# Kernel optimization log

Hardware: AMD Instinct MI355X
Metric: run time of the kernel (lower is better)

The kernel has to match this reference:

```python
import jax, jax.numpy as jnp
import numpy as np

N_NODES = 50000
N_EDGES = 1600000
BN_EPS = 1e-5


def gcn_conv(x, W, b, src, dst, n):
    # PyG GCNConv: h = x @ W; add self-loops; sym-normalized scatter-add; + bias
    h = x @ W                                   # [n, out]
    deg = jnp.zeros((n,), h.dtype).at[dst].add(1.0) + 1.0  # in-degree incl. self-loop
    dinv = jax.lax.rsqrt(deg)                   # deg^{-1/2}
    norm = dinv[src] * dinv[dst]                # per-edge norm
    msg = h[src] * norm[:, None]                # [E, out] gather + scale
    agg = jax.ops.segment_sum(msg, dst, num_segments=n)
    agg = agg + h * (dinv * dinv)[:, None]      # self-loop term: dinv[i]^2 * h[i]
    return agg + b


def bn_eval(x, gamma, beta, mean, var):
    return (x - mean) * jax.lax.rsqrt(var + BN_EPS) * gamma + beta


def setup_inputs() -> dict:
    key = jax.random.key(0)
    ks = jax.random.split(key, 10)
    in_f, c1, c2, out_f = 256, 128, 64, 2
    x = jax.random.normal(ks[0], (N_NODES, in_f), jnp.float32)
    edge_index = jax.random.randint(ks[1], (2, N_EDGES), 0, N_NODES, jnp.int64)
    return {
        "x": x,
        "edge_index": edge_index,
        "W1": jax.random.normal(ks[2], (in_f, c1), jnp.float32) * (1.0 / np.sqrt(in_f)),
        "b1": jnp.zeros((c1,), jnp.float32),
        "W2": jax.random.normal(ks[3], (c1, c2), jnp.float32) * (1.0 / np.sqrt(c1)),
        "b2": jnp.zeros((c2,), jnp.float32),
        "bn1_gamma": jnp.ones((c1,), jnp.float32),
        "bn1_beta": jnp.zeros((c1,), jnp.float32),
        "bn1_mean": jax.random.normal(ks[4], (c1,), jnp.float32) * 0.1,
        "bn1_var": jax.random.uniform(ks[5], (c1,), jnp.float32) + 0.5,
        "bn2_gamma": jnp.ones((c2,), jnp.float32),
        "bn2_beta": jnp.zeros((c2,), jnp.float32),
        "bn2_mean": jax.random.normal(ks[6], (c2,), jnp.float32) * 0.1,
        "bn2_var": jax.random.uniform(ks[7], (c2,), jnp.float32) + 0.5,
        "Wl": jax.random.normal(ks[8], (c2, out_f), jnp.float32) * (1.0 / np.sqrt(c2)),
        "bl": jnp.zeros((out_f,), jnp.float32),
    }


def reference(x, edge_index, W1, b1, W2, b2, bn1_gamma, bn1_beta, bn1_mean, bn1_var,
              bn2_gamma, bn2_beta, bn2_mean, bn2_var, Wl, bl):
    src, dst = edge_index[0], edge_index[1]
    n = x.shape[0]
    h = jax.nn.relu(gcn_conv(x, W1, b1, src, dst, n))
    h = bn_eval(h, bn1_gamma, bn1_beta, bn1_mean, bn1_var)
    # dropout: eval mode -> identity
    h = jax.nn.relu(gcn_conv(h, W2, b2, src, dst, n))
    h = bn_eval(h, bn2_gamma, bn2_beta, bn2_mean, bn2_var)
    return h @ Wl + bl
```

## Files before the change

### kernel.cpp

```cpp
#include <hip/hip_runtime.h>

#define N_NODES 50000
#define N_EDGES 1600000
#define BN_EPS 1e-5f

#define BSH 7
#define BKN 128
#define NB  ((N_NODES + BKN - 1) / BKN)
#define EPT 16
#define EPB (256 * EPT)
#define NEB ((N_EDGES + EPB - 1) / EPB)

typedef unsigned int uint32;
typedef unsigned short ushort16;

__device__ __forceinline__ float bf_lo(uint32 u) { return __uint_as_float(u << 16); }
__device__ __forceinline__ float bf_hi(uint32 u) { return __uint_as_float(u & 0xFFFF0000u); }
__device__ __forceinline__ ushort16 f2bf(float f) {
    uint32 u = __float_as_uint(f);
    u = (u + 0x7FFFu + ((u >> 16) & 1u)) >> 16;
    return (ushort16)u;
}


__global__ __launch_bounds__(256) void bcount_k(const int* __restrict__ ei, int* __restrict__ gcnt) {
    __shared__ int h[NB];
    int t = threadIdx.x;
    for (int i = t; i < NB; i += 256) h[i] = 0;
    __syncthreads();
    int eb = blockIdx.x * EPB;
#pragma unroll
    for (int i = 0; i < EPT; ++i) {
        int e = eb + i * 256 + t;
        if (e < N_EDGES) atomicAdd(&h[ei[N_EDGES + e] >> BSH], 1);
    }
    __syncthreads();
    for (int i = t; i < NB; i += 256) if (h[i]) atomicAdd(&gcnt[i], h[i]);
}

__global__ __launch_bounds__(512) void bscan_k(const int* __restrict__ gcnt, int* __restrict__ gbase,
                                               int* __restrict__ gcursor) {
    __shared__ int wsum[8];
    int t = threadIdx.x;
    int v = (t < NB) ? gcnt[t] : 0;
    int s = v;
#pragma unroll
    for (int d = 1; d < 64; d <<= 1) {
        int n = __shfl_up(s, d);
        if ((t & 63) >= d) s += n;
    }
    if ((t & 63) == 63) wsum[t >> 6] = s;
    __syncthreads();
    if (t < 8) {
        int w = wsum[t];
#pragma unroll
        for (int d = 1; d < 8; d <<= 1) {
            int n = __shfl_up(w, d);
            if (t >= d) w += n;
        }
        wsum[t] = w;
    }
    __syncthreads();
    int wb = (t >> 6) ? wsum[(t >> 6) - 1] : 0;
    int excl = wb + s - v;
    if (t < NB) { gbase[t] = excl; gcursor[t] = excl; }
    if (t == NB - 1) gbase[NB] = excl + v;
}

__global__ __launch_bounds__(256) void bin_k(const int* __restrict__ ei, int* __restrict__ gcursor,
                                             uint32* __restrict__ ebin) {
    __shared__ int hcnt[NB];
    __shared__ int hbase[NB];
    int t = threadIdx.x;
    for (int i = t; i < NB; i += 256) hcnt[i] = 0;
    __syncthreads();
    int sv[EPT], dv[EPT];
    int eb = blockIdx.x * EPB;
#pragma unroll
    for (int i = 0; i < EPT; ++i) {
        int e = eb + i * 256 + t;
        if (e < N_EDGES) {
            sv[i] = ei[e];
            dv[i] = ei[N_EDGES + e];
            atomicAdd(&hcnt[dv[i] >> BSH], 1);
        } else {
            dv[i] = -1;
        }
    }
    __syncthreads();
    for (int i = t; i < NB; i += 256) {
        int c = hcnt[i];
        hbase[i] = c ? atomicAdd(&gcursor[i], c) : 0;
    }
    __syncthreads();
    for (int i = t; i < NB; i += 256) hcnt[i] = 0;
    __syncthreads();
#pragma unroll
    for (int i = 0; i < EPT; ++i) {
        if (dv[i] >= 0) {
            int b = dv[i] >> BSH;
            int off = atomicAdd(&hcnt[b], 1);
            ebin[hbase[b] + off] = (uint32)sv[i] | ((uint32)(dv[i] & (BKN - 1)) << 16);
        }
    }
}

__global__ __launch_bounds__(256) void bsort_k(const int* __restrict__ gbase, const uint32* __restrict__ ebin,
                                               unsigned short* __restrict__ esrc, int* __restrict__ cursor,
                                               float* __restrict__ dinv) {
    __shared__ int hcnt[BKN];
    __shared__ int hoff[BKN];
    __shared__ int wsum2[2];
    int b = blockIdx.x;
    int t = threadIdx.x;
    int ebeg = gbase[b], eend = gbase[b + 1];
    int n0 = b << BSH;
    int nn = min(BKN, N_NODES - n0);
    if (t < BKN) hcnt[t] = 0;
    __syncthreads();
    for (int e = ebeg + t; e < eend; e += 256) atomicAdd(&hcnt[ebin[e] >> 16], 1);
    __syncthreads();
    int v = (t < BKN) ? hcnt[t] : 0;
    int s = v;
#pragma unroll
    for (int d = 1; d < 64; d <<= 1) {
        int x = __shfl_up(s, d);
        if ((t & 63) >= d) s += x;
    }
    if (t < BKN && (t & 63) == 63) wsum2[t >> 6] = s;
    __syncthreads();
    int wb = ((t >> 6) == 1) ? wsum2[0] : 0;
    int incl = wb + s;
    if (t < nn) {
        cursor[n0 + t] = ebeg + incl;
        dinv[n0 + t] = rsqrtf((float)v + 1.0f);
        hoff[t] = ebeg + incl - v;
    }
    __syncthreads();
    for (int e = ebeg + t; e < eend; e += 256) {
        uint32 p = ebin[e];
        int ld = p >> 16;
        int pos = atomicAdd(&hoff[ld], 1);
        esrc[pos] = (unsigned short)(p & 0xFFFFu);
    }
}


__global__ __launch_bounds__(256) void gemm1_k(const float* __restrict__ X, const float* __restrict__ W,
                                               const float* __restrict__ dinv, ushort16* __restrict__ outb) {
    __shared__ float xs[32 * 64];
    __shared__ float ws[32 * 128];
    int tid = threadIdx.x;
    int row0 = blockIdx.x * 64;
    int tx = tid & 15, ty = tid >> 4;
    float acc[4][8] = {};
    for (int k0 = 0; k0 < 256; k0 += 32) {
#pragma unroll
        for (int i = 0; i < 2; ++i) {
            int f = tid + i * 256;
            int r = f >> 3;
            int kg = f & 7;
            int grow = row0 + r;
            float4 v = make_float4(0.f, 0.f, 0.f, 0.f);
            if (grow < N_NODES) v = *(const float4*)&X[grow * 256 + k0 + kg * 4];
            int gc = r >> 2, el = r & 3;
            int pg = gc ^ kg;
            xs[(kg * 4 + 0) * 64 + pg * 4 + el] = v.x;
            xs[(kg * 4 + 1) * 64 + pg * 4 + el] = v.y;
            xs[(kg * 4 + 2) * 64 + pg * 4 + el] = v.z;
            xs[(kg * 4 + 3) * 64 + pg * 4 + el] = v.w;
        }
#pragma unroll
        for (int i = 0; i < 4; ++i) {
            int f = tid + i * 256;
            int r = f >> 5;
            int g = f & 31;
            int p = (g & 1) * 16 + (g >> 1);
            *(float4*)&ws[r * 128 + p * 4] = *(const float4*)&W[(k0 + r) * 128 + g * 4];
        }
        __syncthreads();
#pragma unroll 8
        for (int k = 0; k < 32; ++k) {
            float4 xv = *(const float4*)&xs[k * 64 + ((ty ^ (k >> 2)) << 2)];
            float wv[8];
            *(float4*)&wv[0] = *(const float4*)&ws[k * 128 + tx * 4];
            *(float4*)&wv[4] = *(const float4*)&ws[k * 128 + 64 + tx * 4];
#pragma unroll
            for (int c = 0; c < 8; ++c) {
                acc[0][c] += xv.x * wv[c];
                acc[1][c] += xv.y * wv[c];
                acc[2][c] += xv.z * wv[c];
                acc[3][c] += xv.w * wv[c];
            }
        }
        __syncthreads();
    }
#pragma unroll
    for (int r = 0; r < 4; ++r) {
        int grow = row0 + ty * 4 + r;
        if (grow < N_NODES) {
            float s = dinv[grow];
            uint32 w[4];
#pragma unroll
            for (int c = 0; c < 4; ++c) {
                uint32 lo = (uint32)f2bf(acc[r][2 * c] * s);
                uint32 hi = (uint32)f2bf(acc[r][2 * c + 1] * s);
                w[c] = lo | (hi << 16);
            }
            uint4 o; o.x = w[0]; o.y = w[1]; o.z = w[2]; o.w = w[3];
            *(uint4*)&outb[grow * 128 + tx * 8] = o;
        }
    }
}


__global__ __launch_bounds__(256) void gemm2_k(const float* __restrict__ X, const float* __restrict__ W,
                                               const float* __restrict__ dinv, ushort16* __restrict__ outb) {
    __shared__ float xs[32 * 64];
    __shared__ float ws[32 * 64];
    int tid = threadIdx.x;
    int row0 = blockIdx.x * 64;
    int tx = tid & 15, ty = tid >> 4;
    float acc[4][4] = {};
    for (int k0 = 0; k0 < 128; k0 += 32) {
#pragma unroll
        for (int i = 0; i < 2; ++i) {
            int f = tid + i * 256;
            int r = f >> 3;
            int kg = f & 7;
            int grow = row0 + r;
            float4 v = make_float4(0.f, 0.f, 0.f, 0.f);
            if (grow < N_NODES) v = *(const float4*)&X[grow * 128 + k0 + kg * 4];
            int gc = r >> 2, el = r & 3;
            int pg = gc ^ kg;
            xs[(kg * 4 + 0) * 64 + pg * 4 + el] = v.x;
            xs[(kg * 4 + 1) * 64 + pg * 4 + el] = v.y;
            xs[(kg * 4 + 2) * 64 + pg * 4 + el] = v.z;
            xs[(kg * 4 + 3) * 64 + pg * 4 + el] = v.w;
        }
#pragma unroll
        for (int i = 0; i < 2; ++i) {
            int f = tid + i * 256;
            int r = f >> 4;
            int g = f & 15;
            *(float4*)&ws[r * 64 + g * 4] = *(const float4*)&W[(k0 + r) * 64 + g * 4];
        }
        __syncthreads();
#pragma unroll 8
        for (int k = 0; k < 32; ++k) {
            float4 xv = *(const float4*)&xs[k * 64 + ((ty ^ (k >> 2)) << 2)];
            float4 wv = *(const float4*)&ws[k * 64 + tx * 4];
#pragma unroll
            for (int c = 0; c < 4; ++c) {
                float w = (c == 0) ? wv.x : (c == 1) ? wv.y : (c == 2) ? wv.z : wv.w;
                acc[0][c] += xv.x * w;
                acc[1][c] += xv.y * w;
                acc[2][c] += xv.z * w;
                acc[3][c] += xv.w * w;
            }
        }
        __syncthreads();
    }
#pragma unroll
    for (int r = 0; r < 4; ++r) {
        int grow = row0 + ty * 4 + r;
        if (grow < N_NODES) {
            float s = dinv[grow];
            ushort4 o;
            o.x = f2bf(acc[r][0] * s); o.y = f2bf(acc[r][1] * s);
            o.z = f2bf(acc[r][2] * s); o.w = f2bf(acc[r][3] * s);
            *(ushort4*)&outb[grow * 64 + tx * 4] = o;
        }
    }
}


__global__ __launch_bounds__(256) void gather128_k(const int* __restrict__ cursor, const unsigned short* __restrict__ esrc,
                                                   const ushort16* __restrict__ hsb, const float* __restrict__ dinv,
                                                   const float* __restrict__ bias,
                                                   const float* __restrict__ gamma, const float* __restrict__ beta,
                                                   const float* __restrict__ mean, const float* __restrict__ var,
                                                   float* __restrict__ g1out) {
    int tid = threadIdx.x;
    int n = blockIdx.x * 4 + (tid >> 6);
    int lane = tid & 63;
    int c0 = lane * 2;
    int beg = (n == 0) ? 0 : cursor[n - 1];
    int end = cursor[n];
    float acc0 = 0.f, acc1 = 0.f;
    int e = beg;
    for (; e + 7 < end; e += 8) {
        int s0 = esrc[e + 0], s1 = esrc[e + 1], s2 = esrc[e + 2], s3 = esrc[e + 3];
        int s4 = esrc[e + 4], s5 = esrc[e + 5], s6 = esrc[e + 6], s7 = esrc[e + 7];
        uint32 u0 = *(const uint32*)&hsb[s0 * 128 + c0];
        uint32 u1 = *(const uint32*)&hsb[s1 * 128 + c0];
        uint32 u2 = *(const uint32*)&hsb[s2 * 128 + c0];
        uint32 u3 = *(const uint32*)&hsb[s3 * 128 + c0];
        uint32 u4 = *(const uint32*)&hsb[s4 * 128 + c0];
        uint32 u5 = *(const uint32*)&hsb[s5 * 128 + c0];
        uint32 u6 = *(const uint32*)&hsb[s6 * 128 + c0];
        uint32 u7 = *(const uint32*)&hsb[s7 * 128 + c0];
        acc0 += bf_lo(u0); acc1 += bf_hi(u0);
        acc0 += bf_lo(u1); acc1 += bf_hi(u1);
        acc0 += bf_lo(u2); acc1 += bf_hi(u2);
        acc0 += bf_lo(u3); acc1 += bf_hi(u3);
        acc0 += bf_lo(u4); acc1 += bf_hi(u4);
        acc0 += bf_lo(u5); acc1 += bf_hi(u5);
        acc0 += bf_lo(u6); acc1 += bf_hi(u6);
        acc0 += bf_lo(u7); acc1 += bf_hi(u7);
    }
    for (; e < end; ++e) {
        uint32 u = *(const uint32*)&hsb[(int)esrc[e] * 128 + c0];
        acc0 += bf_lo(u); acc1 += bf_hi(u);
    }
    uint32 us = *(const uint32*)&hsb[n * 128 + c0];
    float di = dinv[n];
    float v0 = di * (acc0 + bf_lo(us)) + bias[c0];
    float v1 = di * (acc1 + bf_hi(us)) + bias[c0 + 1];
    v0 = fmaxf(v0, 0.f);
    v1 = fmaxf(v1, 0.f);
    float g0 = (v0 - mean[c0]) * rsqrtf(var[c0] + BN_EPS) * gamma[c0] + beta[c0];
    float g1 = (v1 - mean[c0 + 1]) * rsqrtf(var[c0 + 1] + BN_EPS) * gamma[c0 + 1] + beta[c0 + 1];
    float2 o; o.x = g0; o.y = g1;
    *(float2*)&g1out[n * 128 + c0] = o;
}

__global__ __launch_bounds__(256) void gather64_k(const int* __restrict__ cursor, const unsigned short* __restrict__ esrc,
                                                  const ushort16* __restrict__ hsb, const float* __restrict__ dinv,
                                                  const float* __restrict__ b2,
                                                  const float* __restrict__ g2, const float* __restrict__ be2,
                                                  const float* __restrict__ m2, const float* __restrict__ v2,
                                                  const float* __restrict__ Wl, const float* __restrict__ bl,
                                                  float* __restrict__ out) {
    int tid = threadIdx.x;
    int n = blockIdx.x * 4 + (tid >> 6);
    int lane = tid & 63;
    int beg = (n == 0) ? 0 : cursor[n - 1];
    int end = cursor[n];
    float acc = 0.f;
    int e = beg;
    for (; e + 7 < end; e += 8) {
        int s0 = esrc[e + 0], s1 = esrc[e + 1], s2 = esrc[e + 2], s3 = esrc[e + 3];
        int s4 = esrc[e + 4], s5 = esrc[e + 5], s6 = esrc[e + 6], s7 = esrc[e + 7];
        float a0 = __uint_as_float(((uint32)hsb[s0 * 64 + lane]) << 16);
        float a1 = __uint_as_float(((uint32)hsb[s1 * 64 + lane]) << 16);
        float a2 = __uint_as_float(((uint32)hsb[s2 * 64 + lane]) << 16);
        float a3 = __uint_as_float(((uint32)hsb[s3 * 64 + lane]) << 16);
        float a4 = __uint_as_float(((uint32)hsb[s4 * 64 + lane]) << 16);
        float a5 = __uint_as_float(((uint32)hsb[s5 * 64 + lane]) << 16);
        float a6 = __uint_as_float(((uint32)hsb[s6 * 64 + lane]) << 16);
        float a7 = __uint_as_float(((uint32)hsb[s7 * 64 + lane]) << 16);
        acc += a0; acc += a1; acc += a2; acc += a3;
        acc += a4; acc += a5; acc += a6; acc += a7;
    }
    for (; e < end; ++e) acc += __uint_as_float(((uint32)hsb[(int)esrc[e] * 64 + lane]) << 16);
    float self = __uint_as_float(((uint32)hsb[n * 64 + lane]) << 16);
    float di = dinv[n];
    float val = di * (acc + self) + b2[lane];
    val = fmaxf(val, 0.f);
    float gg = (val - m2[lane]) * rsqrtf(v2[lane] + BN_EPS) * g2[lane] + be2[lane];
    float p0 = gg * Wl[lane * 2];
    float p1 = gg * Wl[lane * 2 + 1];
#pragma unroll
    for (int d = 32; d > 0; d >>= 1) {
        p0 += __shfl_down(p0, d);
        p1 += __shfl_down(p1, d);
    }
    if (lane == 0) {
        out[n * 2] = p0 + bl[0];
        out[n * 2 + 1] = p1 + bl[1];
    }
}


extern "C" void kernel_launch(void* const* d_in, const int* in_sizes, int n_in,
                              void* d_out, int out_size, void* d_ws, size_t ws_size,
                              hipStream_t stream) {
    const float* x   = (const float*)d_in[0];
    const int*   ei  = (const int*)d_in[1];
    const float* W1  = (const float*)d_in[2];
    const float* b1  = (const float*)d_in[3];
    const float* W2  = (const float*)d_in[4];
    const float* b2  = (const float*)d_in[5];
    const float* g1p = (const float*)d_in[6];
    const float* be1 = (const float*)d_in[7];
    const float* m1  = (const float*)d_in[8];
    const float* v1  = (const float*)d_in[9];
    const float* g2p = (const float*)d_in[10];
    const float* be2 = (const float*)d_in[11];
    const float* m2  = (const float*)d_in[12];
    const float* v2  = (const float*)d_in[13];
    const float* Wl  = (const float*)d_in[14];
    const float* bl  = (const float*)d_in[15];
    float* out = (float*)d_out;

    float* ws = (float*)d_ws;
    float*          dinv    = ws;
    int*            cursor  = (int*)(ws + 50000);
    int*            gcnt    = (int*)(ws + 100000);
    int*            gbase   = (int*)(ws + 100391);
    int*            gcursor = (int*)(ws + 100783);
    uint32*         ebin    = (uint32*)(ws + 101184);
    unsigned short* esrc    = (unsigned short*)(ws + 1701184);
    ushort16*       hs1b    = (ushort16*)(ws + 2501184);
    float*          g1buf   = ws + 5701184;
    ushort16*       hs2b    = (ushort16*)(ws + 12101184);

    hipMemsetAsync(gcnt, 0, NB * sizeof(int), stream);
    bcount_k<<<NEB, 256, 0, stream>>>(ei, gcnt);
    bscan_k<<<1, 512, 0, stream>>>(gcnt, gbase, gcursor);
    bin_k<<<NEB, 256, 0, stream>>>(ei, gcursor, ebin);
    bsort_k<<<NB, 256, 0, stream>>>(gbase, ebin, esrc, cursor, dinv);

    gemm1_k<<<(N_NODES + 63) / 64, 256, 0, stream>>>(x, W1, dinv, hs1b);
    gather128_k<<<(N_NODES + 3) / 4, 256, 0, stream>>>(cursor, esrc, hs1b, dinv, b1, g1p, be1, m1, v1, g1buf);
    gemm2_k<<<(N_NODES + 63) / 64, 256, 0, stream>>>(g1buf, W2, dinv, hs2b);
    gather64_k<<<(N_NODES + 3) / 4, 256, 0, stream>>>(cursor, esrc, hs2b, dinv, b2, g2p, be2, m2, v2, Wl, bl, out);
}
```

Baseline: 344.8 us.

## Use bf16 MFMA for first-layer GEMM with pre-transposed bf16 weights

Replaces the FP32 scalar-FMA tiled GEMM for x@W1 with a bf16 MFMA 16x16x32 kernel. X is converted to bf16 on the fly into LDS, and W1 is transposed and converted to bf16 once per call by a new small kernel. Each block now computes a 128-row by 64-column tile. This cuts compute time on a 50000x256x128 matmul at the cost of bf16 rounding of the inputs. The epilogue switches to scattered 2-byte stores, which may be less efficient than the old vector stores.

```diff
diff --git a/kernel.cpp b/kernel.cpp
--- a/kernel.cpp
+++ b/kernel.cpp
@@ -13,6 +13,8 @@
 
 typedef unsigned int uint32;
 typedef unsigned short ushort16;
+typedef __attribute__((ext_vector_type(8))) short short8v;
+typedef __attribute__((ext_vector_type(4))) float f32x4;
 
 __device__ __forceinline__ float bf_lo(uint32 u) { return __uint_as_float(u << 16); }
 __device__ __forceinline__ float bf_hi(uint32 u) { return __uint_as_float(u & 0xFFFF0000u); }
@@ -146,69 +148,75 @@
 }
 
 
-__global__ __launch_bounds__(256) void gemm1_k(const float* __restrict__ X, const float* __restrict__ W,
+__global__ __launch_bounds__(256) void w1t_k(const float* __restrict__ W, ushort16* __restrict__ WT) {
+    int id = blockIdx.x * 256 + threadIdx.x;
+    if (id >= 128 * 256) return;
+    int c = id >> 8, k = id & 255;
+    WT[c * 256 + k] = f2bf(W[k * 128 + c]);
+}
+
+
+__global__ __launch_bounds__(256) void gemm1_k(const float* __restrict__ X, const ushort16* __restrict__ WT,
                                                const float* __restrict__ dinv, ushort16* __restrict__ outb) {
-    __shared__ float xs[32 * 64];
-    __shared__ float ws[32 * 128];
+    __shared__ uint4 la[512];
+    __shared__ uint4 lb[256];
     int tid = threadIdx.x;
-    int row0 = blockIdx.x * 64;
-    int tx = tid & 15, ty = tid >> 4;
-    float acc[4][8] = {};
+    int w = tid >> 6, l = tid & 63;
+    int row0 = (blockIdx.x >> 1) * 128;
+    int col0 = (blockIdx.x & 1) * 64;
+    f32x4 acc[2][4] = {};
     for (int k0 = 0; k0 < 256; k0 += 32) {
 #pragma unroll
         for (int i = 0; i < 2; ++i) {
-            int f = tid + i * 256;
-            int r = f >> 3;
-            int kg = f & 7;
-            int grow = row0 + r;
-            float4 v = make_float4(0.f, 0.f, 0.f, 0.f);
-            if (grow < N_NODES) v = *(const float4*)&X[grow * 256 + k0 + kg * 4];
-            int gc = r >> 2, el = r & 3;
-            int pg = gc ^ kg;
-            xs[(kg * 4 + 0) * 64 + pg * 4 + el] = v.x;
-            xs[(kg * 4 + 1) * 64 + pg * 4 + el] = v.y;
-            xs[(kg * 4 + 2) * 64 + pg * 4 + el] = v.z;
-            xs[(kg * 4 + 3) * 64 + pg * 4 + el] = v.w;
-        }
-#pragma unroll
-        for (int i = 0; i < 4; ++i) {
-            int f = tid + i * 256;
-            int r = f >> 5;
-            int g = f & 31;
-            int p = (g & 1) * 16 + (g >> 1);
-            *(float4*)&ws[r * 128 + p * 4] = *(const float4*)&W[(k0 + r) * 128 + g * 4];
+            int s = tid + i * 256;
+            int rt = s >> 6, sl = s & 63;
+            int r = row0 + rt * 16 + (sl & 15);
+            int g = sl >> 4;
+            float4 x0 = make_float4(0.f, 0.f, 0.f, 0.f), x1 = x0;
+            if (r < N_NODES) {
+                x0 = *(const float4*)&X[r * 256 + k0 + 4 * g];
+                x1 = *(const float4*)&X[r * 256 + k0 + 16 + 4 * g];
+            }
+            uint4 v;
+            v.x = (uint32)f2bf(x0.x) | ((uint32)f2bf(x0.y) << 16);
+            v.y = (uint32)f2bf(x0.z) | ((uint32)f2bf(x0.w) << 16);
+            v.z = (uint32)f2bf(x1.x) | ((uint32)f2bf(x1.y) << 16);
+            v.w = (uint32)f2bf(x1.z) | ((uint32)f2bf(x1.w) << 16);
+            la[s] = v;
+        }
+        {
+            int ct = tid >> 6, sl = tid & 63;
+            int n = col0 + ct * 16 + (sl & 15);
+            int g = sl >> 4;
+            uint2 lo = *(const uint2*)&WT[n * 256 + k0 + 4 * g];
+            uint2 hi = *(const uint2*)&WT[n * 256 + k0 + 16 + 4 * g];
+            uint4 v; v.x = lo.x; v.y = lo.y; v.z = hi.x; v.w = hi.y;
+            lb[tid] = v;
         }
         __syncthreads();
-#pragma unroll 8
-        for (int k = 0; k < 32; ++k) {
-            float4 xv = *(const float4*)&xs[k * 64 + ((ty ^ (k >> 2)) << 2)];
-            float wv[8];
-            *(float4*)&wv[0] = *(const float4*)&ws[k * 128 + tx * 4];
-            *(float4*)&wv[4] = *(const float4*)&ws[k * 128 + 64 + tx * 4];
-#pragma unroll
-            for (int c = 0; c < 8; ++c) {
-                acc[0][c] += xv.x * wv[c];
-                acc[1][c] += xv.y * wv[c];
-                acc[2][c] += xv.z * wv[c];
-                acc[3][c] += xv.w * wv[c];
+        short8v a0 = *(short8v*)&la[(w * 2 + 0) * 64 + l];
+        short8v a1 = *(short8v*)&la[(w * 2 + 1) * 64 + l];
+#pragma unroll
+        for (int ct = 0; ct < 4; ++ct) {
+            short8v b = *(short8v*)&lb[ct * 64 + l];
+            acc[0][ct] = __builtin_amdgcn_mfma_f32_16x16x32_bf16(a0, b, acc[0][ct], 0, 0, 0);
+            acc[1][ct] = __builtin_amdgcn_mfma_f32_16x16x32_bf16(a1, b, acc[1][ct], 0, 0, 0);
+        }
+        __syncthreads();
+    }
+#pragma unroll
+    for (int i = 0; i < 2; ++i) {
+#pragma unroll
+        for (int q = 0; q < 4; ++q) {
+            int row = row0 + (w * 2 + i) * 16 + (l >> 4) * 4 + q;
+            if (row < N_NODES) {
+                float s = dinv[row];
+#pragma unroll
+                for (int ct = 0; ct < 4; ++ct) {
+                    int col = col0 + ct * 16 + (l & 15);
+                    outb[row * 128 + col] = f2bf(acc[i][ct][q] * s);
+                }
             }
-        }
-        __syncthreads();
-    }
-#pragma unroll
-    for (int r = 0; r < 4; ++r) {
-        int grow = row0 + ty * 4 + r;
-        if (grow < N_NODES) {
-            float s = dinv[grow];
-            uint32 w[4];
-#pragma unroll
-            for (int c = 0; c < 4; ++c) {
-                uint32 lo = (uint32)f2bf(acc[r][2 * c] * s);
-                uint32 hi = (uint32)f2bf(acc[r][2 * c + 1] * s);
-                w[c] = lo | (hi << 16);
-            }
-            uint4 o; o.x = w[0]; o.y = w[1]; o.z = w[2]; o.w = w[3];
-            *(uint4*)&outb[grow * 128 + tx * 8] = o;
         }
     }
 }
@@ -405,14 +413,16 @@
     ushort16*       hs1b    = (ushort16*)(ws + 2501184);
     float*          g1buf   = ws + 5701184;
     ushort16*       hs2b    = (ushort16*)(ws + 12101184);
+    ushort16*       w1t     = (ushort16*)(ws + 13701184);
 
     hipMemsetAsync(gcnt, 0, NB * sizeof(int), stream);
     bcount_k<<<NEB, 256, 0, stream>>>(ei, gcnt);
     bscan_k<<<1, 512, 0, stream>>>(gcnt, gbase, gcursor);
     bin_k<<<NEB, 256, 0, stream>>>(ei, gcursor, ebin);
+    w1t_k<<<128, 256, 0, stream>>>(W1, w1t);
     bsort_k<<<NB, 256, 0, stream>>>(gbase, ebin, esrc, cursor, dinv);
 
-    gemm1_k<<<(N_NODES + 63) / 64, 256, 0, stream>>>(x, W1, dinv, hs1b);
+    gemm1_k<<<782, 256, 0, stream>>>(x, w1t, dinv, hs1b);
     gather128_k<<<(N_NODES + 3) / 4, 256, 0, stream>>>(cursor, esrc, hs1b, dinv, b1, g1p, be1, m1, v1, g1buf);
     gemm2_k<<<(N_NODES + 63) / 64, 256, 0, stream>>>(g1buf, W2, dinv, hs2b);
     gather64_k<<<(N_NODES + 3) / 4, 256, 0, stream>>>(cursor, esrc, hs2b, dinv, b2, g2p, be2, m2, v2, Wl, bl, out);
```

Result: faster. 313.9 us (-9.0%).
